# Kernel tuning notes

Hardware: AMD Instinct MI355X
Metric: run time of the kernel (lower is better)

Reference implementation:

```python
import jax, jax.numpy as jnp
import numpy as np
import math

WINDOW_LEFT = 512   # sliding-window: each query attends to keys in [q-512, q]
WINDOW_RIGHT = 0    # causal
NEG_INF = -1e30


def setup_inputs() -> dict:
    key = jax.random.key(0)
    kq, kk, kv, ks = jax.random.split(key, 4)
    B, S, H, D = 2, 2048, 16, 128
    q = jax.random.normal(kq, (B, S, H, D), dtype=jnp.float32)
    k = jax.random.normal(kk, (B, S, H, D), dtype=jnp.float32)
    v = jax.random.normal(kv, (B, S, H, D), dtype=jnp.float32)
    # geometric-ish ALiBi slopes per head (positive, decaying), like flash-attn
    alibi_slopes = jax.random.uniform(ks, (H,), dtype=jnp.float32, minval=0.001, maxval=0.5)
    return {"q": q, "k": k, "v": v, "alibi_slopes": alibi_slopes}


def reference(q, k, v, alibi_slopes):
    # q,k,v: [B, S, H, D]; alibi_slopes: [H]
    B, S, H, D = q.shape
    scale = 1.0 / math.sqrt(D)
    # scores: [B, H, Sq, Sk]
    scores = jnp.einsum("bqhd,bkhd->bhqk", q, k) * scale
    qi = jnp.arange(S)[:, None]
    ki = jnp.arange(S)[None, :]
    rel = ki - qi  # [Sq, Sk], <=0 for past keys
    # ALiBi bias (equal q/k lengths): -slope * |q - k|
    alibi = -alibi_slopes[:, None, None] * jnp.abs(rel).astype(scores.dtype)  # [H,Sq,Sk]
    scores = scores + alibi[None, :, :, :]
    # causal + sliding-window mask: allow WINDOW_RIGHT future, WINDOW_LEFT past
    mask = (rel <= WINDOW_RIGHT) & (rel >= -WINDOW_LEFT)  # [Sq, Sk]
    scores = jnp.where(mask[None, None, :, :], scores, NEG_INF)
    p = jax.nn.softmax(scores, axis=-1)
    out = jnp.einsum("bhqk,bkhd->bqhd", p, v)
    return out
```

## Files before the change

kernel.cpp:

```cpp
#include <hip/hip_runtime.h>
#include <hip/hip_bf16.h>

typedef __attribute__((ext_vector_type(8))) __bf16 bf16x8;
typedef __attribute__((ext_vector_type(2))) __bf16 bf16x2;
typedef __attribute__((ext_vector_type(4))) float f32x4;

#define MFMA32(a, b, c) __builtin_amdgcn_mfma_f32_16x16x32_bf16((a), (b), (c), 0, 0, 0)

constexpr int Bc = 2, Sc = 2048, Hc = 16, Dc = 128;
constexpr int HD = Hc * Dc;
constexpr int QB = 256;
constexpr float SCALE_L2 = (float)(0.08838834764831844 * 1.4426950408889634);
constexpr float LOG2E = 1.4426950408889634f;
constexpr float NEGF = -30000.0f;
constexpr int KSTR = 2080;

__device__ inline bf16x8 cvt8(f32x4 a, f32x4 b) {
    bf16x8 r;
    r[0]=(__bf16)a[0]; r[1]=(__bf16)a[1]; r[2]=(__bf16)a[2]; r[3]=(__bf16)a[3];
    r[4]=(__bf16)b[0]; r[5]=(__bf16)b[1]; r[6]=(__bf16)b[2]; r[7]=(__bf16)b[3];
    return r;
}

__global__ __launch_bounds__(512, 2) void lumen_attn_kernel(
    const float* __restrict__ Q, const float* __restrict__ K,
    const float* __restrict__ V, const float* __restrict__ SLP,
    float* __restrict__ O)
{
    __shared__ __align__(16) char k_lds[2][64 * 256];
    __shared__ __align__(16) char v_lds[2][8 * KSTR];

    const int tid  = threadIdx.x;
    const int lane = tid & 63;
    const int wid  = tid >> 6;
    const int cl = lane & 15;
    const int kg = lane >> 4;

    const int bid = blockIdx.x;
    const int swz = (bid & 7) * 32 + (bid >> 3);
    const int qb  = (swz & 7) * QB;
    const int bh  = swz >> 3;
    const int h = bh & 15, b = bh >> 4;

    const float slope = SLP[h] * LOG2E;
    const size_t base = (size_t)b * Sc * HD + (size_t)h * Dc;
    const float* qp = Q + base;
    const float* kp = K + base;
    const float* vp = V + base;
    float*       op = O + base;

    const int qw = qb + wid * 32;

    bf16x8 qf[2][4];
    #pragma unroll
    for (int s = 0; s < 2; ++s) {
        const float* qrow = qp + (size_t)(qw + s * 16 + cl) * HD + kg * 8;
        #pragma unroll
        for (int c = 0; c < 4; ++c) {
            f32x4 a = *(const f32x4*)(qrow + c * 32);
            f32x4 bq = *(const f32x4*)(qrow + c * 32 + 4);
            #pragma unroll
            for (int i = 0; i < 4; ++i) { a[i] *= SCALE_L2; bq[i] *= SCALE_L2; }
            qf[s][c] = cvt8(a, bq);
        }
    }

    f32x4 o_acc[2][8];
    #pragma unroll
    for (int s = 0; s < 2; ++s)
        #pragma unroll
        for (int nn = 0; nn < 8; ++nn) o_acc[s][nn] = f32x4{0.f, 0.f, 0.f, 0.f};
    f32x4 ssacc[2];
    ssacc[0] = f32x4{0.f, 0.f, 0.f, 0.f};
    ssacc[1] = f32x4{0.f, 0.f, 0.f, 0.f};

    bf16x8 ones8;
    #pragma unroll
    for (int i = 0; i < 8; ++i) ones8[i] = (__bf16)1.0f;

    int voff[8];
    #pragma unroll
    for (int nn = 0; nn < 8; ++nn) {
        const int d = nn * 16 + cl;
        const int s = (d & ~7) | ((d & 7) ^ ((d >> 3) & 7));
        voff[nn] = s * 16;
    }

    const int kb0    = qb > 512 ? qb - 512 : 0;
    const int kb_end = qb + QB - 64;
    const int NT     = (kb_end - kb0) / 64 + 1;

    const int ktk = tid >> 3;
    const int kd0 = (tid & 7) * 16;
    const int kpos = (2 * ((ktk >> 5) & 1) + ((ktk >> 2) & 1)) * 16
                   + ((ktk >> 3) & 3) * 4 + (ktk & 3);
    const int ksw = (kpos & 15) << 4;
    const int vtk = tid >> 4;
    const int vd0 = (tid & 15) * 8;
    const int va_ = tid & 15;

    f32x4 ra, rb, rc, rd, sa, sb, sc, sd;

    #define LOAD(kbn) do {                                                     \
        const float* kr_ = kp + (size_t)((kbn) + ktk) * HD + kd0;              \
        ra = *(const f32x4*)kr_;        rb = *(const f32x4*)(kr_ + 4);         \
        rc = *(const f32x4*)(kr_ + 8);  rd = *(const f32x4*)(kr_ + 12);        \
        const float* vr_ = vp + (size_t)((kbn) + 2 * vtk) * HD + vd0;          \
        sa = *(const f32x4*)vr_;        sb = *(const f32x4*)(vr_ + 4);         \
        sc = *(const f32x4*)(vr_ + HD); sd = *(const f32x4*)(vr_ + HD + 4);    \
    } while (0)

    #define WRITE(bi) do {                                                     \
        bf16x8 kw0_ = cvt8(ra, rb), kw1_ = cvt8(rc, rd);                       \
        char* kb_ = k_lds[bi] + kpos * 256;                                    \
        *(bf16x8*)(kb_ + ((kd0 * 2) ^ ksw))      = kw0_;                       \
        *(bf16x8*)(kb_ + ((kd0 * 2 + 16) ^ ksw)) = kw1_;                       \
        bf16x8 vw0_ = cvt8(sa, sb), vw1_ = cvt8(sc, sd);                       \
        char* vdst_ = v_lds[bi] + (vtk >> 2) * KSTR + (vtk & 3) * 4;           \
        _Pragma("unroll")                                                      \
        for (int j = 0; j < 8; ++j) {                                          \
            const int s_ = va_ * 8 + (j ^ (va_ & 7));                          \
            bf16x2 pk_; pk_[0] = vw0_[j]; pk_[1] = vw1_[j];                    \
            *(bf16x2*)(vdst_ + s_ * 16) = pk_;                                 \
        }                                                                      \
    } while (0)

    LOAD(kb0);
    WRITE(0);

    for (int i = 0; i < NT; ++i) {
        const int kb  = kb0 + i * 64;
        const int cur = i & 1;
        __syncthreads();

        if (i + 1 < NT) {
            LOAD(kb + 64);
            __builtin_amdgcn_sched_barrier(0);
        }

        if (!(kb > qw + 31 || kb + 63 < qw - 512)) {
            const char* kbuf = k_lds[cur];
            const char* vbuf = v_lds[cur];
            const bool interior = (kb <= qw - 63) && (kb >= qw - 481);

            bf16x8 pa[2][2];
            #pragma unroll
            for (int n = 0; n < 4; ++n) {
                f32x4 s0 = f32x4{0.f, 0.f, 0.f, 0.f};
                f32x4 s1 = f32x4{0.f, 0.f, 0.f, 0.f};
                const char* kbse = kbuf + (n * 16 + cl) * 256;
                const int sw = cl << 4;
                #pragma unroll
                for (int c = 0; c < 4; ++c) {
                    bf16x8 kf = *(const bf16x8*)(kbse + (((c * 32 + kg * 8) * 2) ^ sw));
                    s0 = MFMA32(kf, qf[0][c], s0);
                    s1 = MFMA32(kf, qf[1][c], s1);
                }
                const int keyb = kb + kg * 8 + (n & 1) * 4 + ((n >> 1) << 5);
                if (interior) {
                    const float f0 = (float)((qw + cl) - keyb);
                    #pragma unroll
                    for (int s2 = 0; s2 < 2; ++s2) {
                        const f32x4 sv = s2 ? s1 : s0;
                        const float fq = f0 + (float)(16 * s2);
                        #pragma unroll
                        for (int j = 0; j < 4; ++j) {
                            const float pe = exp2f(fmaf(-slope, fq - (float)j, sv[j]));
                            pa[s2][n >> 1][(n & 1) * 4 + j] = (__bf16)pe;
                        }
                    }
                } else {
                    #pragma unroll
                    for (int s2 = 0; s2 < 2; ++s2) {
                        const f32x4 sv = s2 ? s1 : s0;
                        const int q = qw + s2 * 16 + cl;
                        #pragma unroll
                        for (int j = 0; j < 4; ++j) {
                            const int rel = q - (keyb + j);
                            const float val = ((unsigned)rel <= 512u)
                                              ? fmaf(-slope, (float)rel, sv[j]) : NEGF;
                            const float pe = exp2f(val);
                            pa[s2][n >> 1][(n & 1) * 4 + j] = (__bf16)pe;
                        }
                    }
                }
            }

            ssacc[0] = MFMA32(pa[0][0], ones8, ssacc[0]);
            ssacc[0] = MFMA32(pa[0][1], ones8, ssacc[0]);
            ssacc[1] = MFMA32(pa[1][0], ones8, ssacc[1]);
            ssacc[1] = MFMA32(pa[1][1], ones8, ssacc[1]);

            #pragma unroll
            for (int kk = 0; kk < 2; ++kk) {
                const char* vko = vbuf + (kk * 4 + kg) * KSTR;
                #pragma unroll
                for (int nn = 0; nn < 8; ++nn) {
                    bf16x8 vf = *(const bf16x8*)(vko + voff[nn]);
                    o_acc[0][nn] = MFMA32(pa[0][kk], vf, o_acc[0][nn]);
                    o_acc[1][nn] = MFMA32(pa[1][kk], vf, o_acc[1][nn]);
                }
            }
        }

        if (i + 1 < NT) {
            __builtin_amdgcn_sched_barrier(0);
            WRITE(cur ^ 1);
        }
    }

    const int r0 = kg << 2;
    #pragma unroll
    for (int s = 0; s < 2; ++s) {
        #pragma unroll
        for (int j = 0; j < 4; ++j) {
            const float inv = 1.0f / ssacc[s][j];
            float* orow = op + (size_t)(qw + s * 16 + r0 + j) * HD;
            #pragma unroll
            for (int nn = 0; nn < 8; ++nn)
                orow[nn * 16 + cl] = o_acc[s][nn][j] * inv;
        }
    }
    #undef LOAD
    #undef WRITE
}

extern "C" void kernel_launch(void* const* d_in, const int* in_sizes, int n_in,
                              void* d_out, int out_size, void* d_ws, size_t ws_size,
                              hipStream_t stream) {
    const float* q   = (const float*)d_in[0];
    const float* k   = (const float*)d_in[1];
    const float* v   = (const float*)d_in[2];
    const float* slp = (const float*)d_in[3];
    float* out = (float*)d_out;

    dim3 grid(Bc * Hc * (Sc / QB));
    lumen_attn_kernel<<<grid, dim3(512), 0, stream>>>(q, k, v, slp, out);
}
```

Baseline: 48.61 us.

## Split key range across two blocks and merge partials in combine kernel

Each query block's key tiles are split into two halves handled by separate workgroups, doubling the grid to 512 blocks. Each half writes its unnormalized output in bf16 and its row sums to a workspace. A new combine kernel adds the two halves and normalizes. The aim is to fill the GPU with two blocks per CU instead of one. The cost is extra global traffic and a second launch, plus precision loss from storing partial outputs in bf16.

```diff
diff --git a/kernel.cpp b/kernel.cpp
--- a/kernel.cpp
+++ b/kernel.cpp
@@ -2,6 +2,7 @@
 #include <hip/hip_bf16.h>
 
 typedef __attribute__((ext_vector_type(8))) __bf16 bf16x8;
+typedef __attribute__((ext_vector_type(4))) __bf16 bf16x4;
 typedef __attribute__((ext_vector_type(2))) __bf16 bf16x2;
 typedef __attribute__((ext_vector_type(4))) float f32x4;
 
@@ -10,6 +11,8 @@
 constexpr int Bc = 2, Sc = 2048, Hc = 16, Dc = 128;
 constexpr int HD = Hc * Dc;
 constexpr int QB = 256;
+constexpr int NR = Bc * Sc * Hc;
+constexpr int OUTSZ = Bc * Sc * Hc * Dc;
 constexpr float SCALE_L2 = (float)(0.08838834764831844 * 1.4426950408889634);
 constexpr float LOG2E = 1.4426950408889634f;
 constexpr float NEGF = -30000.0f;
@@ -25,7 +28,8 @@
 __global__ __launch_bounds__(512, 2) void lumen_attn_kernel(
     const float* __restrict__ Q, const float* __restrict__ K,
     const float* __restrict__ V, const float* __restrict__ SLP,
-    float* __restrict__ O)
+    float* __restrict__ O, __bf16* __restrict__ WSO,
+    float* __restrict__ WSS, const int mode)
 {
     __shared__ __align__(16) char k_lds[2][64 * 256];
     __shared__ __align__(16) char v_lds[2][8 * KSTR];
@@ -37,9 +41,15 @@
     const int kg = lane >> 4;
 
     const int bid = blockIdx.x;
-    const int swz = (bid & 7) * 32 + (bid >> 3);
-    const int qb  = (swz & 7) * QB;
-    const int bh  = swz >> 3;
+    int qidx, bh, half;
+    if (mode) {
+        const int swz = (bid & 7) * 64 + (bid >> 3);
+        half = swz & 1; qidx = (swz >> 1) & 7; bh = swz >> 4;
+    } else {
+        const int swz = (bid & 7) * 32 + (bid >> 3);
+        half = 0; qidx = swz & 7; bh = swz >> 3;
+    }
+    const int qb = qidx * QB;
     const int h = bh & 15, b = bh >> 4;
 
     const float slope = SLP[h] * LOG2E;
@@ -47,7 +57,6 @@
     const float* qp = Q + base;
     const float* kp = K + base;
     const float* vp = V + base;
-    float*       op = O + base;
 
     const int qw = qb + wid * 32;
 
@@ -86,9 +95,10 @@
         voff[nn] = s * 16;
     }
 
-    const int kb0    = qb > 512 ? qb - 512 : 0;
-    const int kb_end = qb + QB - 64;
-    const int NT     = (kb_end - kb0) / 64 + 1;
+    const int kb0f   = qb > 512 ? qb - 512 : 0;
+    const int NTf    = (qb + QB - 64 - kb0f) / 64 + 1;
+    const int NT     = mode ? (NTf >> 1) : NTf;
+    const int kb0    = kb0f + (mode ? half * NT * 64 : 0);
 
     const int ktk = tid >> 3;
     const int kd0 = (tid & 7) * 16;
@@ -210,19 +220,59 @@
     }
 
     const int r0 = kg << 2;
-    #pragma unroll
-    for (int s = 0; s < 2; ++s) {
-        #pragma unroll
-        for (int j = 0; j < 4; ++j) {
-            const float inv = 1.0f / ssacc[s][j];
-            float* orow = op + (size_t)(qw + s * 16 + r0 + j) * HD;
-            #pragma unroll
-            for (int nn = 0; nn < 8; ++nn)
-                orow[nn * 16 + cl] = o_acc[s][nn][j] * inv;
+    if (mode) {
+        __bf16* oO = WSO + (size_t)half * OUTSZ + base;
+        float*  sS = WSS + half * NR;
+        #pragma unroll
+        for (int s = 0; s < 2; ++s) {
+            #pragma unroll
+            for (int j = 0; j < 4; ++j) {
+                const int qrow = qw + s * 16 + r0 + j;
+                __bf16* orow = oO + (size_t)qrow * HD;
+                #pragma unroll
+                for (int nn = 0; nn < 8; ++nn)
+                    orow[nn * 16 + cl] = (__bf16)o_acc[s][nn][j];
+                if (cl == 0)
+                    sS[(b * Sc + qrow) * Hc + h] = ssacc[s][j];
+            }
+        }
+    } else {
+        float* op = O + base;
+        #pragma unroll
+        for (int s = 0; s < 2; ++s) {
+            #pragma unroll
+            for (int j = 0; j < 4; ++j) {
+                const float inv = 1.0f / ssacc[s][j];
+                float* orow = op + (size_t)(qw + s * 16 + r0 + j) * HD;
+                #pragma unroll
+                for (int nn = 0; nn < 8; ++nn)
+                    orow[nn * 16 + cl] = o_acc[s][nn][j] * inv;
+            }
         }
     }
     #undef LOAD
     #undef WRITE
+}
+
+__global__ __launch_bounds__(256) void lumen_combine_kernel(
+    const __bf16* __restrict__ WSO, const float* __restrict__ WSS,
+    float* __restrict__ O)
+{
+    const int total4 = OUTSZ / 4;
+    const int stride = gridDim.x * 256;
+    const bf16x4* A = (const bf16x4*)WSO;
+    const bf16x4* B = (const bf16x4*)(WSO + (size_t)OUTSZ);
+    for (int i = blockIdx.x * 256 + threadIdx.x; i < total4; i += stride) {
+        const int row = i >> 5;
+        const float inv = 1.0f / (WSS[row] + WSS[NR + row]);
+        const bf16x4 a = A[i];
+        const bf16x4 c = B[i];
+        f32x4 r;
+        #pragma unroll
+        for (int e = 0; e < 4; ++e)
+            r[e] = ((float)a[e] + (float)c[e]) * inv;
+        ((f32x4*)O)[i] = r;
+    }
 }
 
 extern "C" void kernel_launch(void* const* d_in, const int* in_sizes, int n_in,
@@ -234,6 +284,14 @@
     const float* slp = (const float*)d_in[3];
     float* out = (float*)d_out;
 
-    dim3 grid(Bc * Hc * (Sc / QB));
-    lumen_attn_kernel<<<grid, dim3(512), 0, stream>>>(q, k, v, slp, out);
-}
+    const size_t need = (size_t)2 * OUTSZ * sizeof(__bf16)
+                      + (size_t)2 * NR * sizeof(float);
+    const int mode = (ws_size >= need) ? 1 : 0;
+    __bf16* wsO = (__bf16*)d_ws;
+    float*  wsS = (float*)((char*)d_ws + (size_t)2 * OUTSZ * sizeof(__bf16));
+
+    const int grid = mode ? 512 : 256;
+    lumen_attn_kernel<<<grid, dim3(512), 0, stream>>>(q, k, v, slp, out, wsO, wsS, mode);
+    if (mode)
+        lumen_combine_kernel<<<2048, dim3(256), 0, stream>>>(wsO, wsS, out);
+}
```

After: 67.61 us. 39.1% more time.
